# Optimization experiments

Measured on AMD Instinct MI355X. Metric: run time of the kernel, lower is better.

The kernel has to match this reference:

```python
import jax, jax.numpy as jnp
import numpy as np

ACT_GUARD = 2.0   # 2 ** act_guard_bit (act_guard_bit = 1)
WGT_GUARD = 2.0   # 2 ** weight_guard_bit (weight_guard_bit = 1)


def _ste_round(v):
    # straight-through estimator round (QNMethod.STE)
    return v + jax.lax.stop_gradient(jnp.round(v) - v)


def setup_inputs() -> dict:
    key = jax.random.key(0)
    k_x, k_w, k_b = jax.random.split(key, 3)
    B, S, DIN, DOUT = 4, 2048, 2048, 8192
    ACT_INIT_S, ACT_INIT_Q, LOG_S_INIT = -10.0, 10.0, -8.0
    x = jax.random.normal(k_x, (B, S, DIN), dtype=jnp.float32)
    weight = jax.random.normal(k_w, (DOUT, DIN), dtype=jnp.float32) * 0.02
    bias = jax.random.normal(k_b, (DOUT,), dtype=jnp.float32) * 0.01
    log_act_s = jnp.full((1,), ACT_INIT_S, dtype=jnp.float32)
    log_act_q = jnp.full((1,), ACT_INIT_Q, dtype=jnp.float32)
    act_b = jnp.full((1,), -jnp.exp2(ACT_INIT_Q - 1.0), dtype=jnp.float32)  # -512
    log_wght_s = jnp.full((DOUT, 1), LOG_S_INIT, dtype=jnp.float32)
    return {"x": x, "weight": weight, "bias": bias, "log_act_s": log_act_s,
            "log_act_q": log_act_q, "act_b": act_b, "log_wght_s": log_wght_s}


def reference(x, weight, bias, log_act_s, log_act_q, act_b, log_wght_s):
    # --- activation fake-quant (per-tensor) ---
    s = jnp.exp2(log_act_s)                       # [1]
    q = jnp.exp2(log_act_q)                       # [1]
    zp = jnp.round(act_b / s * ACT_GUARD) / ACT_GUARD * s  # guard-bit rounded zero point
    lo, hi = zp, zp + q - s
    qx = _ste_round((jnp.clip(x, lo, hi) - zp) / s)
    x_dq = qx * s + zp                            # dequantized activations

    # --- weight fake-quant (per-channel over out dim, amin/amax over dim 1) ---
    w_scale = jnp.exp2(log_wght_s)                # [DOUT, 1]
    wmin = jnp.min(weight, axis=1, keepdims=True)
    wmax = jnp.max(weight, axis=1, keepdims=True)
    qwmin = jnp.round(wmin / w_scale * WGT_GUARD) / WGT_GUARD * w_scale
    qwmax = jnp.round(wmax / w_scale * WGT_GUARD) / WGT_GUARD * w_scale
    qw = _ste_round((jnp.clip(weight, qwmin, qwmax) - qwmin) / w_scale)
    w_dq = qw * w_scale + qwmin                   # dequantized weights

    # --- affine: y = x @ W.T + b ---
    return jnp.einsum('bsi,oi->bso', x_dq, w_dq) + bias
```

## Files before the change

### kernel.cpp

```cpp
#include <hip/hip_runtime.h>
#include <hip/hip_bf16.h>


using f16x8 = __attribute__((ext_vector_type(8))) _Float16;
using f32x4 = __attribute__((ext_vector_type(4))) float;

#define AS1 __attribute__((address_space(1)))
#define AS3 __attribute__((address_space(3)))

static __device__ __forceinline__ void gload_lds16(const void* g, void* l) {
    __builtin_amdgcn_global_load_lds((const AS1 void*)g, (AS3 void*)l, 16, 0, 0);
}

__global__ __launch_bounds__(256) void wquant_kernel(
    const float* __restrict__ W, const float* __restrict__ lws,
    _Float16* __restrict__ Wq) {
    constexpr int K = 2048;
    const int row = blockIdx.x;
    const int t = threadIdx.x;
    const float* w = W + (size_t)row * K;

    float4 v0 = ((const float4*)w)[t * 2];
    float4 v1 = ((const float4*)w)[t * 2 + 1];
    float vals[8] = {v0.x, v0.y, v0.z, v0.w, v1.x, v1.y, v1.z, v1.w};

    float mn = vals[0], mx = vals[0];
#pragma unroll
    for (int i = 1; i < 8; ++i) {
        mn = fminf(mn, vals[i]);
        mx = fmaxf(mx, vals[i]);
    }
#pragma unroll
    for (int off = 32; off >= 1; off >>= 1) {
        mn = fminf(mn, __shfl_xor(mn, off));
        mx = fmaxf(mx, __shfl_xor(mx, off));
    }
    __shared__ float smn[4], smx[4];
    if ((t & 63) == 0) { smn[t >> 6] = mn; smx[t >> 6] = mx; }
    __syncthreads();
    mn = fminf(fminf(smn[0], smn[1]), fminf(smn[2], smn[3]));
    mx = fmaxf(fmaxf(smx[0], smx[1]), fmaxf(smx[2], smx[3]));

    const float l = lws[row];
    const float ws = exp2f(l);
    const float rs = exp2f(-l);
    const float qwmin = rintf(mn * rs * 2.0f) * 0.5f * ws;
    const float qwmax = rintf(mx * rs * 2.0f) * 0.5f * ws;

    f16x8 out;
#pragma unroll
    for (int i = 0; i < 8; ++i) {
        float c = fminf(fmaxf(vals[i], qwmin), qwmax);
        float qw = rintf((c - qwmin) * rs);
        out[i] = (_Float16)(qw * ws + qwmin);
    }
    *(f16x8*)&Wq[(size_t)row * K + (size_t)t * 8] = out;
}

__global__ __launch_bounds__(256) void xquant_kernel(
    const float* __restrict__ X,
    const float* __restrict__ las, const float* __restrict__ laq,
    const float* __restrict__ ab, _Float16* __restrict__ Xq) {
    const float ls = las[0], lq = laq[0];
    const float s = exp2f(ls);
    const float rs = exp2f(-ls);
    const float q = exp2f(lq);
    const float zp = rintf(ab[0] * rs * 2.0f) * 0.5f * s;
    const float lo = zp;
    const float hi = (zp + q) - s;

    const size_t base = ((size_t)blockIdx.x * 256 + threadIdx.x) * 8;
    float4 v0 = *(const float4*)&X[base];
    float4 v1 = *(const float4*)&X[base + 4];
    float vals[8] = {v0.x, v0.y, v0.z, v0.w, v1.x, v1.y, v1.z, v1.w};

    f16x8 out;
#pragma unroll
    for (int i = 0; i < 8; ++i) {
        float c = fminf(fmaxf(vals[i], lo), hi);
        float qx = rintf((c - zp) * rs);
        out[i] = (_Float16)(qx * s + zp);
    }
    *(f16x8*)&Xq[base] = out;
}

__global__ __launch_bounds__(512, 2) void gemm_kernel(
    const _Float16* __restrict__ A, const _Float16* __restrict__ B,
    const float* __restrict__ bias, float* __restrict__ C) {
    constexpr int N = 8192, K = 2048;
    constexpr int KT = K / 64;
    constexpr int NBN = N / 256;

    __shared__ char smem[131072];
    char* As = smem;
    char* Bs = smem + 65536;

    const int bid = blockIdx.x;
    const int cpx = gridDim.x >> 3;
    const int swzb = (bid & 7) * cpx + (bid >> 3);
    const int bm = swzb / NBN;
    const int bn = swzb % NBN;

    const int t = threadIdx.x;
    const int lane = t & 63;
    const int wid = t >> 6;
    const int wr = wid >> 2;
    const int wc = wid & 3;
    const int l15 = lane & 15;
    const int lq = lane >> 4;

    const int d0 = t * 16, d1 = (t + 512) * 16;
    const int eoff0 = (d0 >> 6) * K + (((d0 & 63) ^ (((d0 >> 9) & 1) << 5)) >> 1);
    const int eoff1 = (d1 >> 6) * K + (((d1 & 63) ^ (((d1 >> 9) & 1) << 5)) >> 1);
    const _Float16* Agb = A + (size_t)bm * 256 * K;
    const _Float16* Bgb = B + (size_t)bn * 256 * K;

    const int colpart = (lq * 16) ^ ((l15 & 8) << 2);

    f32x4 acc[8][4] = {};
    f16x8 afA[4], afB[4], bf0[4], bf1[4];

#define STAGE(gb, lm, ktSlot, ktSrc, ks) do {                                  \
        const _Float16* _g = (gb) + ((size_t)(ktSrc) * 64 + (ks) * 32);        \
        char* _l = (lm) + ((((ktSlot) & 1) * 2 + (ks)) * 16384);               \
        gload_lds16(_g + eoff0, _l + d0);                                      \
        gload_lds16(_g + eoff1, _l + d1);                                      \
    } while (0)

#define LDA(dst, par, ks, mh) do {                                             \
        const char* _s = As + ((par) * 2 + (ks)) * 16384;                      \
        _Pragma("unroll")                                                      \
        for (int _m = 0; _m < 4; ++_m)                                         \
            dst[_m] = *(const f16x8*)(_s +                                     \
                (wr * 128 + (mh) * 64 + _m * 16 + l15) * 64 + colpart);        \
    } while (0)

#define LDB(dst, par, ks) do {                                                 \
        const char* _s = Bs + ((par) * 2 + (ks)) * 16384;                      \
        _Pragma("unroll")                                                      \
        for (int _n = 0; _n < 4; ++_n)                                         \
            dst[_n] = *(const f16x8*)(_s +                                     \
                (wc * 64 + _n * 16 + l15) * 64 + colpart);                     \
    } while (0)

#define MFMA16(accRow, afv, bfv) do {                                          \
        _Pragma("unroll")                                                      \
        for (int _m = 0; _m < 4; ++_m)                                         \
            _Pragma("unroll")                                                  \
            for (int _n = 0; _n < 4; ++_n)                                     \
                acc[(accRow) + _m][_n] = __builtin_amdgcn_mfma_f32_16x16x32_f16(\
                    afv[_m], bfv[_n], acc[(accRow) + _m][_n], 0, 0, 0);        \
    } while (0)

    STAGE(Bgb, Bs, 0, 0, 0);
    STAGE(Agb, As, 0, 0, 0);
    STAGE(Bgb, Bs, 0, 0, 1);
    STAGE(Agb, As, 0, 0, 1);
    STAGE(Bgb, Bs, 1, 1, 0);
    STAGE(Agb, As, 1, 1, 0);
    STAGE(Bgb, Bs, 1, 1, 1);
    asm volatile("s_waitcnt vmcnt(6)" ::: "memory");
    __builtin_amdgcn_s_barrier();
    LDA(afA, 0, 0, 0);
    LDB(bf0, 0, 0);

    for (int kt = 0; kt < KT; ++kt) {
        const int par = kt & 1;
        const int npar = par ^ 1;
        const int nx = (kt + 1 < KT) ? kt + 1 : KT - 1;
        const int s2 = (kt + 2 < KT) ? kt + 2 : KT - 1;

        LDA(afB, par, 0, 1);
        STAGE(Agb, As, kt + 1, nx, 1);
        __builtin_amdgcn_s_setprio(1);
        MFMA16(0, afA, bf0);
        __builtin_amdgcn_s_setprio(0);
        asm volatile("s_waitcnt vmcnt(8)" ::: "memory");
        __builtin_amdgcn_s_barrier();

        LDA(afA, par, 1, 0);
        LDB(bf1, par, 1);
        STAGE(Bgb, Bs, kt + 2, s2, 0);
        __builtin_amdgcn_s_setprio(1);
        MFMA16(4, afB, bf0);
        __builtin_amdgcn_s_setprio(0);
        __builtin_amdgcn_s_barrier();

        LDA(afB, par, 1, 1);
        STAGE(Agb, As, kt + 2, s2, 0);
        __builtin_amdgcn_s_setprio(1);
        MFMA16(0, afA, bf1);
        __builtin_amdgcn_s_setprio(0);
        asm volatile("s_waitcnt vmcnt(8)" ::: "memory");
        __builtin_amdgcn_s_barrier();

        LDA(afA, npar, 0, 0);
        LDB(bf0, npar, 0);
        STAGE(Bgb, Bs, kt + 2, s2, 1);
        __builtin_amdgcn_s_setprio(1);
        MFMA16(4, afB, bf1);
        __builtin_amdgcn_s_setprio(0);
        __builtin_amdgcn_s_barrier();
    }
#undef STAGE
#undef LDA
#undef LDB
#undef MFMA16

#pragma unroll
    for (int m = 0; m < 8; ++m) {
        const int row = bm * 256 + wr * 128 + m * 16 + lq * 4;
#pragma unroll
        for (int n = 0; n < 4; ++n) {
            const int col = bn * 256 + wc * 64 + n * 16 + l15;
            const float bv = bias[col];
#pragma unroll
            for (int r = 0; r < 4; ++r) {
                C[(size_t)(row + r) * N + col] = acc[m][n][r] + bv;
            }
        }
    }
}

extern "C" void kernel_launch(void* const* d_in, const int* in_sizes, int n_in,
                              void* d_out, int out_size, void* d_ws, size_t ws_size,
                              hipStream_t stream) {
    const float* x    = (const float*)d_in[0];
    const float* w    = (const float*)d_in[1];
    const float* bias = (const float*)d_in[2];
    const float* las  = (const float*)d_in[3];
    const float* laq  = (const float*)d_in[4];
    const float* ab   = (const float*)d_in[5];
    const float* lws  = (const float*)d_in[6];
    float* out = (float*)d_out;

    constexpr size_t MK = (size_t)8192 * 2048;
    _Float16* xq = (_Float16*)d_ws;
    _Float16* wq = (_Float16*)((char*)d_ws + MK * sizeof(_Float16));

    xquant_kernel<<<8192, 256, 0, stream>>>(x, las, laq, ab, xq);
    wquant_kernel<<<8192, 256, 0, stream>>>(w, lws, wq);
    gemm_kernel<<<1024, 512, 0, stream>>>(xq, wq, bias, out);
}
```

Measured before the change: 331.3 us.

## Restructure GEMM main loop into 8-wave quadrant schedule with 128-row LDS tiles

Reorganizes the LDS layout so each stage holds a 128-row by 64-k half tile (128-byte rows with a new XOR swizzle) instead of 256 rows by 32-k. The main loop is unrolled by two k-tiles into a four-phase schedule in which each phase loads one A or B fragment quarter, issues one global-to-LDS stage, and then runs 16 MFMAs. It adds explicit lgkmcnt waits and extra barriers. The aim is better overlap of global loads, LDS reads and MFMA, with fewer LDS reads per MFMA, at the cost of more synchronization and intricate prefetch indexing.

```diff
diff --git a/kernel.cpp b/kernel.cpp
--- a/kernel.cpp
+++ b/kernel.cpp
@@ -92,8 +92,6 @@
     constexpr int NBN = N / 256;
 
     __shared__ char smem[131072];
-    char* As = smem;
-    char* Bs = smem + 65536;
 
     const int bid = blockIdx.x;
     const int cpx = gridDim.x >> 3;
@@ -109,103 +107,126 @@
     const int l15 = lane & 15;
     const int lq = lane >> 4;
 
-    const int d0 = t * 16, d1 = (t + 512) * 16;
-    const int eoff0 = (d0 >> 6) * K + (((d0 & 63) ^ (((d0 >> 9) & 1) << 5)) >> 1);
-    const int eoff1 = (d1 >> 6) * K + (((d1 & 63) ^ (((d1 >> 9) & 1) << 5)) >> 1);
+    const int d0 = t * 16, d1 = d0 + 8192;
+    const int r0 = d0 >> 7, c0 = (((d0 & 127) ^ (((d0 >> 9) & 1) << 5)) >> 1);
+    const int r1 = d1 >> 7, c1 = (((d1 & 127) ^ (((d1 >> 9) & 1) << 5)) >> 1);
     const _Float16* Agb = A + (size_t)bm * 256 * K;
     const _Float16* Bgb = B + (size_t)bn * 256 * K;
 
-    const int colpart = (lq * 16) ^ ((l15 & 8) << 2);
+    const int cp = (lq * 16) ^ ((l15 & 4) << 3);
 
     f32x4 acc[8][4] = {};
-    f16x8 afA[4], afB[4], bf0[4], bf1[4];
-
-#define STAGE(gb, lm, ktSlot, ktSrc, ks) do {                                  \
-        const _Float16* _g = (gb) + ((size_t)(ktSrc) * 64 + (ks) * 32);        \
-        char* _l = (lm) + ((((ktSlot) & 1) * 2 + (ks)) * 16384);               \
-        gload_lds16(_g + eoff0, _l + d0);                                      \
-        gload_lds16(_g + eoff1, _l + d1);                                      \
-    } while (0)
-
-#define LDA(dst, par, ks, mh) do {                                             \
-        const char* _s = As + ((par) * 2 + (ks)) * 16384;                      \
+    f16x8 fA0[4][2], fA1[4][2], fB0[2][2], fB1[2][2];
+
+#define STAGE(GB, RO, DBS, H, KS) do {                                         \
+        const _Float16* _g = (GB) + (size_t)((H) * 128) * K + (size_t)(KS) * 64;\
+        char* _l = smem + (RO) + ((DBS) * 2 + (H)) * 16384;                    \
+        gload_lds16(_g + (size_t)r0 * K + c0, _l + d0);                        \
+        gload_lds16(_g + (size_t)r1 * K + c1, _l + d1);                        \
+    } while (0)
+
+#define LDAF(dst, DBv, MLO) do {                                               \
+        const char* _s = smem + ((DBv) * 2 + wr) * 16384 + l15 * 128 + cp;     \
         _Pragma("unroll")                                                      \
-        for (int _m = 0; _m < 4; ++_m)                                         \
-            dst[_m] = *(const f16x8*)(_s +                                     \
-                (wr * 128 + (mh) * 64 + _m * 16 + l15) * 64 + colpart);        \
-    } while (0)
-
-#define LDB(dst, par, ks) do {                                                 \
-        const char* _s = Bs + ((par) * 2 + (ks)) * 16384;                      \
+        for (int _m = 0; _m < 4; ++_m) {                                       \
+            dst[_m][0] = *(const f16x8*)(_s + ((MLO) + _m) * 2048);            \
+            dst[_m][1] = *(const f16x8*)(_s + ((MLO) + _m) * 2048 + 64);       \
+        }                                                                      \
+    } while (0)
+
+#define LDBF(dst, DBv, NLO) do {                                               \
+        const char* _s = smem + 65536 + ((DBv) * 2 + (wc >> 1)) * 16384 +      \
+                         (wc & 1) * 8192 + l15 * 128 + cp;                     \
         _Pragma("unroll")                                                      \
-        for (int _n = 0; _n < 4; ++_n)                                         \
-            dst[_n] = *(const f16x8*)(_s +                                     \
-                (wc * 64 + _n * 16 + l15) * 64 + colpart);                     \
-    } while (0)
-
-#define MFMA16(accRow, afv, bfv) do {                                          \
+        for (int _n = 0; _n < 2; ++_n) {                                       \
+            dst[_n][0] = *(const f16x8*)(_s + ((NLO) + _n) * 2048);            \
+            dst[_n][1] = *(const f16x8*)(_s + ((NLO) + _n) * 2048 + 64);       \
+        }                                                                      \
+    } while (0)
+
+#define QMFMA(MLO, NLO, AF, BF) do {                                           \
         _Pragma("unroll")                                                      \
         for (int _m = 0; _m < 4; ++_m)                                         \
             _Pragma("unroll")                                                  \
-            for (int _n = 0; _n < 4; ++_n)                                     \
-                acc[(accRow) + _m][_n] = __builtin_amdgcn_mfma_f32_16x16x32_f16(\
-                    afv[_m], bfv[_n], acc[(accRow) + _m][_n], 0, 0, 0);        \
-    } while (0)
-
-    STAGE(Bgb, Bs, 0, 0, 0);
-    STAGE(Agb, As, 0, 0, 0);
-    STAGE(Bgb, Bs, 0, 0, 1);
-    STAGE(Agb, As, 0, 0, 1);
-    STAGE(Bgb, Bs, 1, 1, 0);
-    STAGE(Agb, As, 1, 1, 0);
-    STAGE(Bgb, Bs, 1, 1, 1);
-    asm volatile("s_waitcnt vmcnt(6)" ::: "memory");
+            for (int _n = 0; _n < 2; ++_n) {                                   \
+                f32x4 _c = acc[(MLO) + _m][(NLO) + _n];                        \
+                _c = __builtin_amdgcn_mfma_f32_16x16x32_f16(                   \
+                    AF[_m][0], BF[_n][0], _c, 0, 0, 0);                        \
+                _c = __builtin_amdgcn_mfma_f32_16x16x32_f16(                   \
+                    AF[_m][1], BF[_n][1], _c, 0, 0, 0);                        \
+                acc[(MLO) + _m][(NLO) + _n] = _c;                              \
+            }                                                                  \
+    } while (0)
+
+#define HALFITER(DBv, S1, S2, S3, S4, VMW) do {                                \
+                                                          \
+        LDAF(fA0, DBv, 0); LDBF(fB0, DBv, 0);                                  \
+        S1;                                                                    \
+        asm volatile("s_waitcnt lgkmcnt(8)" ::: "memory");                     \
+        __builtin_amdgcn_s_barrier();                                          \
+        asm volatile("s_waitcnt lgkmcnt(0)" ::: "memory");                     \
+        __builtin_amdgcn_s_setprio(1);                                         \
+        QMFMA(0, 0, fA0, fB0);                                                 \
+        __builtin_amdgcn_s_setprio(0);                                         \
+        __builtin_amdgcn_s_barrier();                                          \
+                                                           \
+        LDBF(fB1, DBv, 2);                                                     \
+        S2;                                                                    \
+        __builtin_amdgcn_s_barrier();                                          \
+        asm volatile("s_waitcnt lgkmcnt(0)" ::: "memory");                     \
+        __builtin_amdgcn_s_setprio(1);                                         \
+        QMFMA(0, 2, fA0, fB1);                                                 \
+        __builtin_amdgcn_s_setprio(0);                                         \
+        __builtin_amdgcn_s_barrier();                                          \
+                                                           \
+        LDAF(fA1, DBv, 4);                                                     \
+        S3;                                                                    \
+        __builtin_amdgcn_s_barrier();                                          \
+        asm volatile("s_waitcnt lgkmcnt(0)" ::: "memory");                     \
+        __builtin_amdgcn_s_setprio(1);                                         \
+        QMFMA(4, 2, fA1, fB1);                                                 \
+        __builtin_amdgcn_s_setprio(0);                                         \
+        __builtin_amdgcn_s_barrier();                                          \
+                                                           \
+        S4;                                                                    \
+        __builtin_amdgcn_s_barrier();                                          \
+        __builtin_amdgcn_s_setprio(1);                                         \
+        QMFMA(4, 0, fA1, fB0);                                                 \
+        __builtin_amdgcn_s_setprio(0);                                         \
+        asm volatile("s_waitcnt vmcnt(" #VMW ")" ::: "memory");                \
+        __builtin_amdgcn_s_barrier();                                          \
+    } while (0)
+
+    STAGE(Bgb, 65536, 0, 0, 0);
+    STAGE(Agb, 0,     0, 0, 0);
+    STAGE(Agb, 0,     0, 1, 0);
+    STAGE(Bgb, 65536, 0, 1, 0);
+    STAGE(Bgb, 65536, 1, 0, 1);
+    STAGE(Bgb, 65536, 1, 1, 1);
+    asm volatile("s_waitcnt vmcnt(4)" ::: "memory");
     __builtin_amdgcn_s_barrier();
-    LDA(afA, 0, 0, 0);
-    LDB(bf0, 0, 0);
-
-    for (int kt = 0; kt < KT; ++kt) {
-        const int par = kt & 1;
-        const int npar = par ^ 1;
-        const int nx = (kt + 1 < KT) ? kt + 1 : KT - 1;
-        const int s2 = (kt + 2 < KT) ? kt + 2 : KT - 1;
-
-        LDA(afB, par, 0, 1);
-        STAGE(Agb, As, kt + 1, nx, 1);
-        __builtin_amdgcn_s_setprio(1);
-        MFMA16(0, afA, bf0);
-        __builtin_amdgcn_s_setprio(0);
-        asm volatile("s_waitcnt vmcnt(8)" ::: "memory");
-        __builtin_amdgcn_s_barrier();
-
-        LDA(afA, par, 1, 0);
-        LDB(bf1, par, 1);
-        STAGE(Bgb, Bs, kt + 2, s2, 0);
-        __builtin_amdgcn_s_setprio(1);
-        MFMA16(4, afB, bf0);
-        __builtin_amdgcn_s_setprio(0);
-        __builtin_amdgcn_s_barrier();
-
-        LDA(afB, par, 1, 1);
-        STAGE(Agb, As, kt + 2, s2, 0);
-        __builtin_amdgcn_s_setprio(1);
-        MFMA16(0, afA, bf1);
-        __builtin_amdgcn_s_setprio(0);
-        asm volatile("s_waitcnt vmcnt(8)" ::: "memory");
-        __builtin_amdgcn_s_barrier();
-
-        LDA(afA, npar, 0, 0);
-        LDB(bf0, npar, 0);
-        STAGE(Bgb, Bs, kt + 2, s2, 1);
-        __builtin_amdgcn_s_setprio(1);
-        MFMA16(4, afB, bf1);
-        __builtin_amdgcn_s_setprio(0);
-        __builtin_amdgcn_s_barrier();
-    }
+
+    for (int it = 0; it < KT / 2; ++it) {
+        const int b  = 2 * it + 1;
+        const int aN = (2 * it + 2 < KT) ? 2 * it + 2 : KT - 2;
+        const int bN = (2 * it + 3 < KT) ? 2 * it + 3 : KT - 1;
+
+        HALFITER(0,
+                 STAGE(Agb, 0,     1, 0, b),
+                 STAGE(Agb, 0,     1, 1, b),
+                 STAGE(Bgb, 65536, 0, 0, aN),
+                 STAGE(Agb, 0,     0, 0, aN), 4);
+        HALFITER(1,
+                 STAGE(Agb, 0,     0, 1, aN),
+                 STAGE(Bgb, 65536, 0, 1, aN),
+                 STAGE(Bgb, 65536, 1, 0, bN),
+                 STAGE(Bgb, 65536, 1, 1, bN), 4);
+    }
+#undef HALFITER
+#undef QMFMA
+#undef LDBF
+#undef LDAF
 #undef STAGE
-#undef LDA
-#undef LDB
-#undef MFMA16
 
 #pragma unroll
     for (int m = 0; m < 8; ++m) {
```

After: 300.8 us. 1.1x faster.
